# Kernel tuning notes

Measured on AMD Instinct MI355X. Metric: run time of the kernel, lower is better.

Reference implementation:

```python
import jax, jax.numpy as jnp
import numpy as np

N_NODES = 50000
N_EDGES = 800000
D_IN = 64
D_OUT = 64


def setup_inputs() -> dict:
    key = jax.random.key(0)
    k1, k2, k3, k4 = jax.random.split(key, 4)
    x = jax.random.normal(k1, (N_NODES, D_IN), dtype=jnp.float32)
    edge_index = jax.random.randint(k2, (2, N_EDGES), 0, N_NODES, dtype=jnp.int64)
    # GCNConv params: glorot weight [in, out], zero bias [out]
    limit = np.sqrt(6.0 / (D_IN + D_OUT)).astype(np.float32)
    W = jax.random.uniform(k3, (D_IN, D_OUT), minval=-limit, maxval=limit, dtype=jnp.float32)
    b = jnp.zeros((D_OUT,), dtype=jnp.float32)
    return {"x": x, "edge_index": edge_index, "W": W, "b": b}


def reference(x, edge_index, W, b):
    # GCNConv forward: linear transform, add self-loops, symmetric normalization,
    # scatter-add aggregation, bias.
    N = x.shape[0]
    xw = x @ W  # [N, D_OUT]

    self_loops = jnp.arange(N, dtype=edge_index.dtype)
    src = jnp.concatenate([edge_index[0], self_loops])  # source / neighbor j
    dst = jnp.concatenate([edge_index[1], self_loops])  # target / center i

    ones = jnp.ones_like(dst, dtype=xw.dtype)
    deg = jax.ops.segment_sum(ones, dst, num_segments=N)  # in-degree incl. self-loop
    deg_inv_sqrt = jnp.where(deg > 0, jax.lax.rsqrt(deg), 0.0)
    norm = deg_inv_sqrt[src] * deg_inv_sqrt[dst]  # [E+N]

    msgs = xw[src] * norm[:, None]  # gather + scale, [E+N, D_OUT]
    out = jax.ops.segment_sum(msgs, dst, num_segments=N)  # scatter-add
    return out + b
```

## Files before the change

kernel.cpp:

```cpp
#include <hip/hip_runtime.h>

constexpr int N_NODES = 50000;
constexpr int N_EDGES = 800000;
constexpr int D = 64;
constexpr int CAP = 64;
constexpr int NODES_PER_XCD = N_NODES / 8;
constexpr int NPB = 32;

constexpr int OFF_CUR  = 0;
constexpr int OFF_DISV = 50016;
constexpr int OFF_BKT  = 100032;
constexpr int OFF_XWF  = 3300032;
constexpr int OFF_XW2  = 6500032;

__device__ __forceinline__ float lo_bf(unsigned int u) {
    union { unsigned int x; float f; } c; c.x = u << 16; return c.f;
}
__device__ __forceinline__ float hi_bf(unsigned int u) {
    union { unsigned int x; float f; } c; c.x = u & 0xFFFF0000u; return c.f;
}
__device__ __forceinline__ unsigned short f2bf(float f) {
    union { float f; unsigned int u; } c; c.f = f;
    unsigned int r = (c.u + 0x7FFFu + ((c.u >> 16) & 1u)) >> 16;
    return (unsigned short)r;
}

__global__ void k_xw(const float* __restrict__ x, const float* __restrict__ W,
                     float* __restrict__ xwf, int* __restrict__ cur) {
    __shared__ float sW[D * D];
    __shared__ float sx[NPB][D];
    int t = threadIdx.x;
    int zi = blockIdx.x * 256 + t;
    if (zi < N_NODES) cur[zi] = 0;
    for (int i = t; i < D * D; i += 256) sW[i] = W[i];
    int local = t >> 6;
    int j     = t & 63;
    int base  = blockIdx.x * NPB;
    #pragma unroll
    for (int r = 0; r < NPB / 4; ++r) {
        int node = base + r * 4 + local;
        sx[r * 4 + local][j] = (node < N_NODES) ? x[node * D + j] : 0.0f;
    }
    __syncthreads();
    float acc[NPB / 4];
    #pragma unroll
    for (int r = 0; r < NPB / 4; ++r) acc[r] = 0.0f;
    for (int k = 0; k < D; ++k) {
        float wk = sW[k * D + j];
        #pragma unroll
        for (int r = 0; r < NPB / 4; ++r) acc[r] += sx[r * 4 + local][k] * wk;
    }
    #pragma unroll
    for (int r = 0; r < NPB / 4; ++r) {
        int node = base + r * 4 + local;
        if (node < N_NODES) xwf[node * D + j] = acc[r];
    }
}

__global__ void k_place(const int4* __restrict__ src4, const int4* __restrict__ dst4,
                        int* __restrict__ cur, int* __restrict__ bucket) {
    int g   = blockIdx.x & 7;
    int bg  = blockIdx.x >> 3;
    int nbg = gridDim.x >> 3;
    int lo = g * NODES_PER_XCD, hi = lo + NODES_PER_XCD;
    int nq = N_EDGES / 4;
    for (int e = bg * blockDim.x + threadIdx.x; e < nq; e += nbg * blockDim.x) {
        int4 d = dst4[e];
        bool mx = (d.x >= lo) & (d.x < hi);
        bool my = (d.y >= lo) & (d.y < hi);
        bool mz = (d.z >= lo) & (d.z < hi);
        bool mw = (d.w >= lo) & (d.w < hi);
        if (mx | my | mz | mw) {
            int4 s = src4[e];
            if (mx) { int p = atomicAdd(&cur[d.x], 1); if (p < CAP) bucket[d.x * CAP + p] = s.x; }
            if (my) { int p = atomicAdd(&cur[d.y], 1); if (p < CAP) bucket[d.y * CAP + p] = s.y; }
            if (mz) { int p = atomicAdd(&cur[d.z], 1); if (p < CAP) bucket[d.z * CAP + p] = s.z; }
            if (mw) { int p = atomicAdd(&cur[d.w], 1); if (p < CAP) bucket[d.w * CAP + p] = s.w; }
        }
    }
}

__global__ void k_scale(const int* __restrict__ cur, const float4* __restrict__ xwf4,
                        unsigned short* __restrict__ xw2, float* __restrict__ disv) {
    int t = blockIdx.x * blockDim.x + threadIdx.x;
    if (t >= N_NODES * D / 4) return;
    int base = t * 4;
    int i = base >> 6;
    float dis = rsqrtf((float)(cur[i] + 1));
    if ((base & 63) == 0) disv[i] = dis;
    float4 v = xwf4[t];
    ushort4 o;
    o.x = f2bf(dis * v.x); o.y = f2bf(dis * v.y);
    o.z = f2bf(dis * v.z); o.w = f2bf(dis * v.w);
    *reinterpret_cast<ushort4*>(xw2 + base) = o;
}

__global__ void k_agg(const int* __restrict__ cur, const int* __restrict__ bucket,
                      const unsigned short* __restrict__ xw2,
                      const float* __restrict__ disv,
                      const float* __restrict__ b, float* __restrict__ out) {
    int t = threadIdx.x;
    int w = t >> 6, l = t & 63, g = l >> 3, q = l & 7;
    int i = blockIdx.x * 4 + w;
    if (i >= N_NODES) return;
    int deg = cur[i];
    if (deg > CAP) deg = CAP;
    float a0 = 0.f, a1 = 0.f, a2 = 0.f, a3 = 0.f,
          a4 = 0.f, a5 = 0.f, a6 = 0.f, a7 = 0.f;
    const int* bkt = bucket + i * CAP;
    for (int k = g; k < deg; k += 8) {
        int s = bkt[k];
        uint4 v = *reinterpret_cast<const uint4*>(xw2 + s * D + q * 8);
        a0 += lo_bf(v.x); a1 += hi_bf(v.x);
        a2 += lo_bf(v.y); a3 += hi_bf(v.y);
        a4 += lo_bf(v.z); a5 += hi_bf(v.z);
        a6 += lo_bf(v.w); a7 += hi_bf(v.w);
    }
    a0 += __shfl_xor(a0, 8); a0 += __shfl_xor(a0, 16); a0 += __shfl_xor(a0, 32);
    a1 += __shfl_xor(a1, 8); a1 += __shfl_xor(a1, 16); a1 += __shfl_xor(a1, 32);
    a2 += __shfl_xor(a2, 8); a2 += __shfl_xor(a2, 16); a2 += __shfl_xor(a2, 32);
    a3 += __shfl_xor(a3, 8); a3 += __shfl_xor(a3, 16); a3 += __shfl_xor(a3, 32);
    a4 += __shfl_xor(a4, 8); a4 += __shfl_xor(a4, 16); a4 += __shfl_xor(a4, 32);
    a5 += __shfl_xor(a5, 8); a5 += __shfl_xor(a5, 16); a5 += __shfl_xor(a5, 32);
    a6 += __shfl_xor(a6, 8); a6 += __shfl_xor(a6, 16); a6 += __shfl_xor(a6, 32);
    a7 += __shfl_xor(a7, 8); a7 += __shfl_xor(a7, 16); a7 += __shfl_xor(a7, 32);
    if (g == 0) {
        float di = disv[i];
        uint4 sv = *reinterpret_cast<const uint4*>(xw2 + i * D + q * 8);
        float4 bv0 = *reinterpret_cast<const float4*>(b + q * 8);
        float4 bv1 = *reinterpret_cast<const float4*>(b + q * 8 + 4);
        float4 r0, r1;
        r0.x = di * (a0 + lo_bf(sv.x)) + bv0.x;
        r0.y = di * (a1 + hi_bf(sv.x)) + bv0.y;
        r0.z = di * (a2 + lo_bf(sv.y)) + bv0.z;
        r0.w = di * (a3 + hi_bf(sv.y)) + bv0.w;
        r1.x = di * (a4 + lo_bf(sv.z)) + bv1.x;
        r1.y = di * (a5 + hi_bf(sv.z)) + bv1.y;
        r1.z = di * (a6 + lo_bf(sv.w)) + bv1.z;
        r1.w = di * (a7 + hi_bf(sv.w)) + bv1.w;
        *reinterpret_cast<float4*>(out + i * D + q * 8)     = r0;
        *reinterpret_cast<float4*>(out + i * D + q * 8 + 4) = r1;
    }
}

extern "C" void kernel_launch(void* const* d_in, const int* in_sizes, int n_in,
                              void* d_out, int out_size, void* d_ws, size_t ws_size,
                              hipStream_t stream) {
    const float* x    = (const float*)d_in[0];
    const int*   edge = (const int*)d_in[1];
    const float* W    = (const float*)d_in[2];
    const float* b    = (const float*)d_in[3];
    float* out = (float*)d_out;

    const int4* src4 = (const int4*)edge;
    const int4* dst4 = (const int4*)(edge + N_EDGES);

    int* ws_i = (int*)d_ws;
    int*   cur    = ws_i + OFF_CUR;
    float* disv   = (float*)(ws_i + OFF_DISV);
    int*   bucket = ws_i + OFF_BKT;
    float* xwf    = (float*)(ws_i + OFF_XWF);
    unsigned short* xw2 = (unsigned short*)(ws_i + OFF_XW2);

    k_xw   <<<(N_NODES + NPB - 1) / NPB, 256, 0, stream>>>(x, W, xwf, cur);
    k_place<<<8 * 104, 256, 0, stream>>>(src4, dst4, cur, bucket);
    k_scale<<<(N_NODES * D / 4 + 255) / 256, 256, 0, stream>>>(cur, (const float4*)xwf, xw2, disv);
    k_agg  <<<(N_NODES + 3) / 4, 256, 0, stream>>>(cur, bucket, xw2, disv, b, out);
}
```

Baseline: 156.9 us.

## Fuse four GCN stages into one persistent cooperative kernel with grid syncs

Merges the xW matmul, edge bucketing, degree scaling and aggregation kernels into one cooperative persistent kernel. Grid-wide syncs separate the stages, and each stage loops over its work with a grid-stride. The goal is to remove three kernel launch gaps and their tail effects. In exchange the grid is capped at 1024 blocks, the matmul tile shrinks to 16 nodes, grid.sync adds its own cost, and occupancy is fixed for all phases.

After: 552.0 us. +251.7%, slower.

```diff
diff --git a/kernel.cpp b/kernel.cpp
--- a/kernel.cpp
+++ b/kernel.cpp
@@ -1,11 +1,13 @@
 #include <hip/hip_runtime.h>
+#include <hip/hip_cooperative_groups.h>
+
+namespace cg = cooperative_groups;
 
 constexpr int N_NODES = 50000;
 constexpr int N_EDGES = 800000;
 constexpr int D = 64;
 constexpr int CAP = 64;
 constexpr int NODES_PER_XCD = N_NODES / 8;
-constexpr int NPB = 32;
 
 constexpr int OFF_CUR  = 0;
 constexpr int OFF_DISV = 50016;
@@ -25,121 +27,133 @@
     return (unsigned short)r;
 }
 
-__global__ void k_xw(const float* __restrict__ x, const float* __restrict__ W,
-                     float* __restrict__ xwf, int* __restrict__ cur) {
+__global__ __launch_bounds__(256, 4)
+void k_fused(const float* __restrict__ x, const float* __restrict__ W,
+             const int4* __restrict__ src4, const int4* __restrict__ dst4,
+             const float* __restrict__ b, float* __restrict__ out,
+             int* __restrict__ cur, int* __restrict__ bucket,
+             float* __restrict__ xwf, unsigned short* __restrict__ xw2,
+             float* __restrict__ disv) {
+    cg::grid_group grid = cg::this_grid();
     __shared__ float sW[D * D];
-    __shared__ float sx[NPB][D];
-    int t = threadIdx.x;
-    int zi = blockIdx.x * 256 + t;
-    if (zi < N_NODES) cur[zi] = 0;
+    __shared__ float sx[16][D];
+    const int t   = threadIdx.x;
+    const int bid = blockIdx.x;
+    const int nb  = gridDim.x;
+
     for (int i = t; i < D * D; i += 256) sW[i] = W[i];
-    int local = t >> 6;
-    int j     = t & 63;
-    int base  = blockIdx.x * NPB;
-    #pragma unroll
-    for (int r = 0; r < NPB / 4; ++r) {
-        int node = base + r * 4 + local;
-        sx[r * 4 + local][j] = (node < N_NODES) ? x[node * D + j] : 0.0f;
-    }
-    __syncthreads();
-    float acc[NPB / 4];
-    #pragma unroll
-    for (int r = 0; r < NPB / 4; ++r) acc[r] = 0.0f;
-    for (int k = 0; k < D; ++k) {
-        float wk = sW[k * D + j];
+    for (int i = bid * 256 + t; i < N_NODES; i += nb * 256) cur[i] = 0;
+
+    const int local = t >> 6;
+    const int j     = t & 63;
+    const int NT    = (N_NODES + 15) / 16;
+    for (int tile = bid; tile < NT; tile += nb) {
+        int base = tile * 16;
+        __syncthreads();
         #pragma unroll
-        for (int r = 0; r < NPB / 4; ++r) acc[r] += sx[r * 4 + local][k] * wk;
-    }
-    #pragma unroll
-    for (int r = 0; r < NPB / 4; ++r) {
-        int node = base + r * 4 + local;
-        if (node < N_NODES) xwf[node * D + j] = acc[r];
-    }
-}
-
-__global__ void k_place(const int4* __restrict__ src4, const int4* __restrict__ dst4,
-                        int* __restrict__ cur, int* __restrict__ bucket) {
-    int g   = blockIdx.x & 7;
-    int bg  = blockIdx.x >> 3;
-    int nbg = gridDim.x >> 3;
-    int lo = g * NODES_PER_XCD, hi = lo + NODES_PER_XCD;
-    int nq = N_EDGES / 4;
-    for (int e = bg * blockDim.x + threadIdx.x; e < nq; e += nbg * blockDim.x) {
-        int4 d = dst4[e];
-        bool mx = (d.x >= lo) & (d.x < hi);
-        bool my = (d.y >= lo) & (d.y < hi);
-        bool mz = (d.z >= lo) & (d.z < hi);
-        bool mw = (d.w >= lo) & (d.w < hi);
-        if (mx | my | mz | mw) {
-            int4 s = src4[e];
-            if (mx) { int p = atomicAdd(&cur[d.x], 1); if (p < CAP) bucket[d.x * CAP + p] = s.x; }
-            if (my) { int p = atomicAdd(&cur[d.y], 1); if (p < CAP) bucket[d.y * CAP + p] = s.y; }
-            if (mz) { int p = atomicAdd(&cur[d.z], 1); if (p < CAP) bucket[d.z * CAP + p] = s.z; }
-            if (mw) { int p = atomicAdd(&cur[d.w], 1); if (p < CAP) bucket[d.w * CAP + p] = s.w; }
+        for (int r = 0; r < 4; ++r) {
+            int node = base + r * 4 + local;
+            sx[r * 4 + local][j] = (node < N_NODES) ? x[node * D + j] : 0.0f;
+        }
+        __syncthreads();
+        float acc[4] = {0.f, 0.f, 0.f, 0.f};
+        for (int k = 0; k < D; ++k) {
+            float wk = sW[k * D + j];
+            #pragma unroll
+            for (int r = 0; r < 4; ++r) acc[r] += sx[r * 4 + local][k] * wk;
+        }
+        #pragma unroll
+        for (int r = 0; r < 4; ++r) {
+            int node = base + r * 4 + local;
+            if (node < N_NODES) xwf[node * D + j] = acc[r];
         }
     }
-}
+    grid.sync();
 
-__global__ void k_scale(const int* __restrict__ cur, const float4* __restrict__ xwf4,
-                        unsigned short* __restrict__ xw2, float* __restrict__ disv) {
-    int t = blockIdx.x * blockDim.x + threadIdx.x;
-    if (t >= N_NODES * D / 4) return;
-    int base = t * 4;
-    int i = base >> 6;
-    float dis = rsqrtf((float)(cur[i] + 1));
-    if ((base & 63) == 0) disv[i] = dis;
-    float4 v = xwf4[t];
-    ushort4 o;
-    o.x = f2bf(dis * v.x); o.y = f2bf(dis * v.y);
-    o.z = f2bf(dis * v.z); o.w = f2bf(dis * v.w);
-    *reinterpret_cast<ushort4*>(xw2 + base) = o;
-}
+    {
+        int g   = bid & 7;
+        int bg  = bid >> 3;
+        int nbg = nb >> 3;
+        int lo = g * NODES_PER_XCD, hi = lo + NODES_PER_XCD;
+        int nq = N_EDGES / 4;
+        for (int e = bg * 256 + t; e < nq; e += nbg * 256) {
+            int4 d = dst4[e];
+            bool mx = (d.x >= lo) & (d.x < hi);
+            bool my = (d.y >= lo) & (d.y < hi);
+            bool mz = (d.z >= lo) & (d.z < hi);
+            bool mw = (d.w >= lo) & (d.w < hi);
+            if (mx | my | mz | mw) {
+                int4 s = src4[e];
+                if (mx) { int p = atomicAdd(&cur[d.x], 1); if (p < CAP) bucket[d.x * CAP + p] = s.x; }
+                if (my) { int p = atomicAdd(&cur[d.y], 1); if (p < CAP) bucket[d.y * CAP + p] = s.y; }
+                if (mz) { int p = atomicAdd(&cur[d.z], 1); if (p < CAP) bucket[d.z * CAP + p] = s.z; }
+                if (mw) { int p = atomicAdd(&cur[d.w], 1); if (p < CAP) bucket[d.w * CAP + p] = s.w; }
+            }
+        }
+    }
+    grid.sync();
 
-__global__ void k_agg(const int* __restrict__ cur, const int* __restrict__ bucket,
-                      const unsigned short* __restrict__ xw2,
-                      const float* __restrict__ disv,
-                      const float* __restrict__ b, float* __restrict__ out) {
-    int t = threadIdx.x;
-    int w = t >> 6, l = t & 63, g = l >> 3, q = l & 7;
-    int i = blockIdx.x * 4 + w;
-    if (i >= N_NODES) return;
-    int deg = cur[i];
-    if (deg > CAP) deg = CAP;
-    float a0 = 0.f, a1 = 0.f, a2 = 0.f, a3 = 0.f,
-          a4 = 0.f, a5 = 0.f, a6 = 0.f, a7 = 0.f;
-    const int* bkt = bucket + i * CAP;
-    for (int k = g; k < deg; k += 8) {
-        int s = bkt[k];
-        uint4 v = *reinterpret_cast<const uint4*>(xw2 + s * D + q * 8);
-        a0 += lo_bf(v.x); a1 += hi_bf(v.x);
-        a2 += lo_bf(v.y); a3 += hi_bf(v.y);
-        a4 += lo_bf(v.z); a5 += hi_bf(v.z);
-        a6 += lo_bf(v.w); a7 += hi_bf(v.w);
+    {
+        const float4* xwf4 = (const float4*)xwf;
+        int nq = N_NODES * D / 4;
+        for (int u = bid * 256 + t; u < nq; u += nb * 256) {
+            int base = u * 4;
+            int i = base >> 6;
+            float dis = rsqrtf((float)(cur[i] + 1));
+            if ((base & 63) == 0) disv[i] = dis;
+            float4 v = xwf4[u];
+            ushort4 o;
+            o.x = f2bf(dis * v.x); o.y = f2bf(dis * v.y);
+            o.z = f2bf(dis * v.z); o.w = f2bf(dis * v.w);
+            *reinterpret_cast<ushort4*>(xw2 + base) = o;
+        }
     }
-    a0 += __shfl_xor(a0, 8); a0 += __shfl_xor(a0, 16); a0 += __shfl_xor(a0, 32);
-    a1 += __shfl_xor(a1, 8); a1 += __shfl_xor(a1, 16); a1 += __shfl_xor(a1, 32);
-    a2 += __shfl_xor(a2, 8); a2 += __shfl_xor(a2, 16); a2 += __shfl_xor(a2, 32);
-    a3 += __shfl_xor(a3, 8); a3 += __shfl_xor(a3, 16); a3 += __shfl_xor(a3, 32);
-    a4 += __shfl_xor(a4, 8); a4 += __shfl_xor(a4, 16); a4 += __shfl_xor(a4, 32);
-    a5 += __shfl_xor(a5, 8); a5 += __shfl_xor(a5, 16); a5 += __shfl_xor(a5, 32);
-    a6 += __shfl_xor(a6, 8); a6 += __shfl_xor(a6, 16); a6 += __shfl_xor(a6, 32);
-    a7 += __shfl_xor(a7, 8); a7 += __shfl_xor(a7, 16); a7 += __shfl_xor(a7, 32);
-    if (g == 0) {
-        float di = disv[i];
-        uint4 sv = *reinterpret_cast<const uint4*>(xw2 + i * D + q * 8);
-        float4 bv0 = *reinterpret_cast<const float4*>(b + q * 8);
-        float4 bv1 = *reinterpret_cast<const float4*>(b + q * 8 + 4);
-        float4 r0, r1;
-        r0.x = di * (a0 + lo_bf(sv.x)) + bv0.x;
-        r0.y = di * (a1 + hi_bf(sv.x)) + bv0.y;
-        r0.z = di * (a2 + lo_bf(sv.y)) + bv0.z;
-        r0.w = di * (a3 + hi_bf(sv.y)) + bv0.w;
-        r1.x = di * (a4 + lo_bf(sv.z)) + bv1.x;
-        r1.y = di * (a5 + hi_bf(sv.z)) + bv1.y;
-        r1.z = di * (a6 + lo_bf(sv.w)) + bv1.z;
-        r1.w = di * (a7 + hi_bf(sv.w)) + bv1.w;
-        *reinterpret_cast<float4*>(out + i * D + q * 8)     = r0;
-        *reinterpret_cast<float4*>(out + i * D + q * 8 + 4) = r1;
+    grid.sync();
+
+    {
+        int wave = bid * 4 + (t >> 6);
+        int nw   = nb * 4;
+        int l = t & 63, g = l >> 3, q = l & 7;
+        for (int i = wave; i < N_NODES; i += nw) {
+            int deg = cur[i];
+            if (deg > CAP) deg = CAP;
+            float a0 = 0.f, a1 = 0.f, a2 = 0.f, a3 = 0.f,
+                  a4 = 0.f, a5 = 0.f, a6 = 0.f, a7 = 0.f;
+            const int* bkt = bucket + i * CAP;
+            for (int k = g; k < deg; k += 8) {
+                int s = bkt[k];
+                uint4 v = *reinterpret_cast<const uint4*>(xw2 + s * D + q * 8);
+                a0 += lo_bf(v.x); a1 += hi_bf(v.x);
+                a2 += lo_bf(v.y); a3 += hi_bf(v.y);
+                a4 += lo_bf(v.z); a5 += hi_bf(v.z);
+                a6 += lo_bf(v.w); a7 += hi_bf(v.w);
+            }
+            a0 += __shfl_xor(a0, 8); a0 += __shfl_xor(a0, 16); a0 += __shfl_xor(a0, 32);
+            a1 += __shfl_xor(a1, 8); a1 += __shfl_xor(a1, 16); a1 += __shfl_xor(a1, 32);
+            a2 += __shfl_xor(a2, 8); a2 += __shfl_xor(a2, 16); a2 += __shfl_xor(a2, 32);
+            a3 += __shfl_xor(a3, 8); a3 += __shfl_xor(a3, 16); a3 += __shfl_xor(a3, 32);
+            a4 += __shfl_xor(a4, 8); a4 += __shfl_xor(a4, 16); a4 += __shfl_xor(a4, 32);
+            a5 += __shfl_xor(a5, 8); a5 += __shfl_xor(a5, 16); a5 += __shfl_xor(a5, 32);
+            a6 += __shfl_xor(a6, 8); a6 += __shfl_xor(a6, 16); a6 += __shfl_xor(a6, 32);
+            a7 += __shfl_xor(a7, 8); a7 += __shfl_xor(a7, 16); a7 += __shfl_xor(a7, 32);
+            if (g == 0) {
+                float di = disv[i];
+                uint4 sv = *reinterpret_cast<const uint4*>(xw2 + i * D + q * 8);
+                float4 bv0 = *reinterpret_cast<const float4*>(b + q * 8);
+                float4 bv1 = *reinterpret_cast<const float4*>(b + q * 8 + 4);
+                float4 r0, r1;
+                r0.x = di * (a0 + lo_bf(sv.x)) + bv0.x;
+                r0.y = di * (a1 + hi_bf(sv.x)) + bv0.y;
+                r0.z = di * (a2 + lo_bf(sv.y)) + bv0.z;
+                r0.w = di * (a3 + hi_bf(sv.y)) + bv0.w;
+                r1.x = di * (a4 + lo_bf(sv.z)) + bv1.x;
+                r1.y = di * (a5 + hi_bf(sv.z)) + bv1.y;
+                r1.z = di * (a6 + lo_bf(sv.w)) + bv1.z;
+                r1.w = di * (a7 + hi_bf(sv.w)) + bv1.w;
+                *reinterpret_cast<float4*>(out + i * D + q * 8)     = r0;
+                *reinterpret_cast<float4*>(out + i * D + q * 8 + 4) = r1;
+            }
+        }
     }
 }
 
@@ -162,8 +176,16 @@
     float* xwf    = (float*)(ws_i + OFF_XWF);
     unsigned short* xw2 = (unsigned short*)(ws_i + OFF_XW2);
 
-    k_xw   <<<(N_NODES + NPB - 1) / NPB, 256, 0, stream>>>(x, W, xwf, cur);
-    k_place<<<8 * 104, 256, 0, stream>>>(src4, dst4, cur, bucket);
-    k_scale<<<(N_NODES * D / 4 + 255) / 256, 256, 0, stream>>>(cur, (const float4*)xwf, xw2, disv);
-    k_agg  <<<(N_NODES + 3) / 4, 256, 0, stream>>>(cur, bucket, xw2, disv, b, out);
+    int maxb = 4;
+    hipOccupancyMaxActiveBlocksPerMultiprocessor(&maxb, (const void*)k_fused, 256, 0);
+    int grid = maxb * 256;
+    if (grid > 1024) grid = 1024;
+    grid &= ~7;
+    if (grid < 8) grid = 8;
+
+    void* args[] = { (void*)&x, (void*)&W, (void*)&src4, (void*)&dst4,
+                     (void*)&b, (void*)&out, (void*)&cur, (void*)&bucket,
+                     (void*)&xwf, (void*)&xw2, (void*)&disv };
+    hipLaunchCooperativeKernel((const void*)k_fused, dim3(grid), dim3(256),
+                               args, 0, stream);
 }
```

## Fuse edge placement with XW GEMM and fold degree scaling into aggregation

Applied to the files above, without the earlier changes.

Merges the edge bucketing and the x@W transform into one launch, with block ranges split between the two roles. The XW result goes straight to bf16, which removes the fp32 intermediate buffer and the separate scale kernel. Source-side normalization moves into the aggregation loop as a per-neighbor rsqrt of cur[s], and a memset replaces the in-kernel zeroing of cur. The trade is an extra random 4-byte gather per edge in aggregation, plus computing the center-node degree from the value clamped to CAP, which differs from the reference only for nodes with more than 64 incoming edges.

Measured after the change: 146.2 us. 6.9% less time.

```diff
diff --git a/kernel.cpp b/kernel.cpp
--- a/kernel.cpp
+++ b/kernel.cpp
@@ -6,12 +6,12 @@
 constexpr int CAP = 64;
 constexpr int NODES_PER_XCD = N_NODES / 8;
 constexpr int NPB = 32;
+constexpr int PLACE_B = 8 * 104;
+constexpr int XW_B = (N_NODES + NPB - 1) / NPB;
 
-constexpr int OFF_CUR  = 0;
-constexpr int OFF_DISV = 50016;
-constexpr int OFF_BKT  = 100032;
-constexpr int OFF_XWF  = 3300032;
-constexpr int OFF_XW2  = 6500032;
+constexpr int OFF_CUR = 0;
+constexpr int OFF_BKT = 50016;
+constexpr int OFF_XW2 = 3250016;
 
 __device__ __forceinline__ float lo_bf(unsigned int u) {
     union { unsigned int x; float f; } c; c.x = u << 16; return c.f;
@@ -25,79 +25,63 @@
     return (unsigned short)r;
 }
 
-__global__ void k_xw(const float* __restrict__ x, const float* __restrict__ W,
-                     float* __restrict__ xwf, int* __restrict__ cur) {
-    __shared__ float sW[D * D];
-    __shared__ float sx[NPB][D];
-    int t = threadIdx.x;
-    int zi = blockIdx.x * 256 + t;
-    if (zi < N_NODES) cur[zi] = 0;
-    for (int i = t; i < D * D; i += 256) sW[i] = W[i];
-    int local = t >> 6;
-    int j     = t & 63;
-    int base  = blockIdx.x * NPB;
-    #pragma unroll
-    for (int r = 0; r < NPB / 4; ++r) {
-        int node = base + r * 4 + local;
-        sx[r * 4 + local][j] = (node < N_NODES) ? x[node * D + j] : 0.0f;
-    }
-    __syncthreads();
-    float acc[NPB / 4];
-    #pragma unroll
-    for (int r = 0; r < NPB / 4; ++r) acc[r] = 0.0f;
-    for (int k = 0; k < D; ++k) {
-        float wk = sW[k * D + j];
+__global__ __launch_bounds__(256)
+void k_build(const float* __restrict__ x, const float* __restrict__ W,
+             const int4* __restrict__ src4, const int4* __restrict__ dst4,
+             int* __restrict__ cur, int* __restrict__ bucket,
+             unsigned short* __restrict__ xw2) {
+    const int t = threadIdx.x;
+    if (blockIdx.x < PLACE_B) {
+        int g   = blockIdx.x & 7;
+        int bg  = blockIdx.x >> 3;
+        int nbg = PLACE_B >> 3;
+        int lo = g * NODES_PER_XCD, hi = lo + NODES_PER_XCD;
+        int nq = N_EDGES / 4;
+        for (int e = bg * 256 + t; e < nq; e += nbg * 256) {
+            int4 d = dst4[e];
+            bool mx = (d.x >= lo) & (d.x < hi);
+            bool my = (d.y >= lo) & (d.y < hi);
+            bool mz = (d.z >= lo) & (d.z < hi);
+            bool mw = (d.w >= lo) & (d.w < hi);
+            if (mx | my | mz | mw) {
+                int4 s = src4[e];
+                if (mx) { int p = atomicAdd(&cur[d.x], 1); if (p < CAP) bucket[d.x * CAP + p] = s.x; }
+                if (my) { int p = atomicAdd(&cur[d.y], 1); if (p < CAP) bucket[d.y * CAP + p] = s.y; }
+                if (mz) { int p = atomicAdd(&cur[d.z], 1); if (p < CAP) bucket[d.z * CAP + p] = s.z; }
+                if (mw) { int p = atomicAdd(&cur[d.w], 1); if (p < CAP) bucket[d.w * CAP + p] = s.w; }
+            }
+        }
+    } else {
+        __shared__ float sW[D * D];
+        __shared__ float sx[NPB][D];
+        for (int i = t; i < D * D; i += 256) sW[i] = W[i];
+        int local = t >> 6;
+        int j     = t & 63;
+        int base  = (blockIdx.x - PLACE_B) * NPB;
         #pragma unroll
-        for (int r = 0; r < NPB / 4; ++r) acc[r] += sx[r * 4 + local][k] * wk;
-    }
-    #pragma unroll
-    for (int r = 0; r < NPB / 4; ++r) {
-        int node = base + r * 4 + local;
-        if (node < N_NODES) xwf[node * D + j] = acc[r];
-    }
-}
-
-__global__ void k_place(const int4* __restrict__ src4, const int4* __restrict__ dst4,
-                        int* __restrict__ cur, int* __restrict__ bucket) {
-    int g   = blockIdx.x & 7;
-    int bg  = blockIdx.x >> 3;
-    int nbg = gridDim.x >> 3;
-    int lo = g * NODES_PER_XCD, hi = lo + NODES_PER_XCD;
-    int nq = N_EDGES / 4;
-    for (int e = bg * blockDim.x + threadIdx.x; e < nq; e += nbg * blockDim.x) {
-        int4 d = dst4[e];
-        bool mx = (d.x >= lo) & (d.x < hi);
-        bool my = (d.y >= lo) & (d.y < hi);
-        bool mz = (d.z >= lo) & (d.z < hi);
-        bool mw = (d.w >= lo) & (d.w < hi);
-        if (mx | my | mz | mw) {
-            int4 s = src4[e];
-            if (mx) { int p = atomicAdd(&cur[d.x], 1); if (p < CAP) bucket[d.x * CAP + p] = s.x; }
-            if (my) { int p = atomicAdd(&cur[d.y], 1); if (p < CAP) bucket[d.y * CAP + p] = s.y; }
-            if (mz) { int p = atomicAdd(&cur[d.z], 1); if (p < CAP) bucket[d.z * CAP + p] = s.z; }
-            if (mw) { int p = atomicAdd(&cur[d.w], 1); if (p < CAP) bucket[d.w * CAP + p] = s.w; }
+        for (int r = 0; r < NPB / 4; ++r) {
+            int node = base + r * 4 + local;
+            sx[r * 4 + local][j] = (node < N_NODES) ? x[node * D + j] : 0.0f;
+        }
+        __syncthreads();
+        float acc[NPB / 4];
+        #pragma unroll
+        for (int r = 0; r < NPB / 4; ++r) acc[r] = 0.0f;
+        for (int k = 0; k < D; ++k) {
+            float wk = sW[k * D + j];
+            #pragma unroll
+            for (int r = 0; r < NPB / 4; ++r) acc[r] += sx[r * 4 + local][k] * wk;
+        }
+        #pragma unroll
+        for (int r = 0; r < NPB / 4; ++r) {
+            int node = base + r * 4 + local;
+            if (node < N_NODES) xw2[node * D + j] = f2bf(acc[r]);
         }
     }
 }
 
-__global__ void k_scale(const int* __restrict__ cur, const float4* __restrict__ xwf4,
-                        unsigned short* __restrict__ xw2, float* __restrict__ disv) {
-    int t = blockIdx.x * blockDim.x + threadIdx.x;
-    if (t >= N_NODES * D / 4) return;
-    int base = t * 4;
-    int i = base >> 6;
-    float dis = rsqrtf((float)(cur[i] + 1));
-    if ((base & 63) == 0) disv[i] = dis;
-    float4 v = xwf4[t];
-    ushort4 o;
-    o.x = f2bf(dis * v.x); o.y = f2bf(dis * v.y);
-    o.z = f2bf(dis * v.z); o.w = f2bf(dis * v.w);
-    *reinterpret_cast<ushort4*>(xw2 + base) = o;
-}
-
 __global__ void k_agg(const int* __restrict__ cur, const int* __restrict__ bucket,
                       const unsigned short* __restrict__ xw2,
-                      const float* __restrict__ disv,
                       const float* __restrict__ b, float* __restrict__ out) {
     int t = threadIdx.x;
     int w = t >> 6, l = t & 63, g = l >> 3, q = l & 7;
@@ -110,11 +94,12 @@
     const int* bkt = bucket + i * CAP;
     for (int k = g; k < deg; k += 8) {
         int s = bkt[k];
+        float ds = rsqrtf((float)(cur[s] + 1));
         uint4 v = *reinterpret_cast<const uint4*>(xw2 + s * D + q * 8);
-        a0 += lo_bf(v.x); a1 += hi_bf(v.x);
-        a2 += lo_bf(v.y); a3 += hi_bf(v.y);
-        a4 += lo_bf(v.z); a5 += hi_bf(v.z);
-        a6 += lo_bf(v.w); a7 += hi_bf(v.w);
+        a0 += ds * lo_bf(v.x); a1 += ds * hi_bf(v.x);
+        a2 += ds * lo_bf(v.y); a3 += ds * hi_bf(v.y);
+        a4 += ds * lo_bf(v.z); a5 += ds * hi_bf(v.z);
+        a6 += ds * lo_bf(v.w); a7 += ds * hi_bf(v.w);
     }
     a0 += __shfl_xor(a0, 8); a0 += __shfl_xor(a0, 16); a0 += __shfl_xor(a0, 32);
     a1 += __shfl_xor(a1, 8); a1 += __shfl_xor(a1, 16); a1 += __shfl_xor(a1, 32);
@@ -125,19 +110,19 @@
     a6 += __shfl_xor(a6, 8); a6 += __shfl_xor(a6, 16); a6 += __shfl_xor(a6, 32);
     a7 += __shfl_xor(a7, 8); a7 += __shfl_xor(a7, 16); a7 += __shfl_xor(a7, 32);
     if (g == 0) {
-        float di = disv[i];
+        float di = rsqrtf((float)(deg + 1));
         uint4 sv = *reinterpret_cast<const uint4*>(xw2 + i * D + q * 8);
         float4 bv0 = *reinterpret_cast<const float4*>(b + q * 8);
         float4 bv1 = *reinterpret_cast<const float4*>(b + q * 8 + 4);
         float4 r0, r1;
-        r0.x = di * (a0 + lo_bf(sv.x)) + bv0.x;
-        r0.y = di * (a1 + hi_bf(sv.x)) + bv0.y;
-        r0.z = di * (a2 + lo_bf(sv.y)) + bv0.z;
-        r0.w = di * (a3 + hi_bf(sv.y)) + bv0.w;
-        r1.x = di * (a4 + lo_bf(sv.z)) + bv1.x;
-        r1.y = di * (a5 + hi_bf(sv.z)) + bv1.y;
-        r1.z = di * (a6 + lo_bf(sv.w)) + bv1.z;
-        r1.w = di * (a7 + hi_bf(sv.w)) + bv1.w;
+        r0.x = di * (a0 + di * lo_bf(sv.x)) + bv0.x;
+        r0.y = di * (a1 + di * hi_bf(sv.x)) + bv0.y;
+        r0.z = di * (a2 + di * lo_bf(sv.y)) + bv0.z;
+        r0.w = di * (a3 + di * hi_bf(sv.y)) + bv0.w;
+        r1.x = di * (a4 + di * lo_bf(sv.z)) + bv1.x;
+        r1.y = di * (a5 + di * hi_bf(sv.z)) + bv1.y;
+        r1.z = di * (a6 + di * lo_bf(sv.w)) + bv1.z;
+        r1.w = di * (a7 + di * hi_bf(sv.w)) + bv1.w;
         *reinterpret_cast<float4*>(out + i * D + q * 8)     = r0;
         *reinterpret_cast<float4*>(out + i * D + q * 8 + 4) = r1;
     }
@@ -156,14 +141,11 @@
     const int4* dst4 = (const int4*)(edge + N_EDGES);
 
     int* ws_i = (int*)d_ws;
-    int*   cur    = ws_i + OFF_CUR;
-    float* disv   = (float*)(ws_i + OFF_DISV);
-    int*   bucket = ws_i + OFF_BKT;
-    float* xwf    = (float*)(ws_i + OFF_XWF);
+    int* cur    = ws_i + OFF_CUR;
+    int* bucket = ws_i + OFF_BKT;
     unsigned short* xw2 = (unsigned short*)(ws_i + OFF_XW2);
 
-    k_xw   <<<(N_NODES + NPB - 1) / NPB, 256, 0, stream>>>(x, W, xwf, cur);
-    k_place<<<8 * 104, 256, 0, stream>>>(src4, dst4, cur, bucket);
-    k_scale<<<(N_NODES * D / 4 + 255) / 256, 256, 0, stream>>>(cur, (const float4*)xwf, xw2, disv);
-    k_agg  <<<(N_NODES + 3) / 4, 256, 0, stream>>>(cur, bucket, xw2, disv, b, out);
+    hipMemsetAsync(cur, 0, N_NODES * sizeof(int), stream);
+    k_build<<<PLACE_B + XW_B, 256, 0, stream>>>(x, W, src4, dst4, cur, bucket, xw2);
+    k_agg  <<<(N_NODES + 3) / 4, 256, 0, stream>>>(cur, bucket, xw2, b, out);
 }
```
